# Performance work log

Measured on AMD Instinct MI355X. Metric: run time of the kernel, lower is better.

Reference implementation:

```python
import jax, jax.numpy as jnp
import numpy as np
import math

IN_FEATURES = 4096
OUT_FEATURES = 4096
NUM_COMPONENTS = 256
TWO_PI = 2.0 * math.pi


def setup_inputs() -> dict:
    key = jax.random.key(0)
    k1, k2, k3, k4 = jax.random.split(key, 4)
    x = jax.random.normal(k1, (4096, IN_FEATURES), dtype=jnp.float32)
    mus = jax.random.uniform(k2, (NUM_COMPONENTS, 2), dtype=jnp.float32)
    log_vars = -3.0 - jax.random.uniform(k3, (NUM_COMPONENTS, 2), dtype=jnp.float32)
    weights = jax.random.uniform(k4, (NUM_COMPONENTS,), dtype=jnp.float32) / NUM_COMPONENTS
    return {"x": x, "mus": mus, "log_vars": log_vars, "weights": weights}


def reference(x, mus, log_vars, weights):
    in_features = x.shape[1]
    x_in_idx = jnp.linspace(0.0, 1.0, in_features, dtype=jnp.float32)    # [I]
    x_out_idx = jnp.linspace(0.0, 1.0, OUT_FEATURES, dtype=jnp.float32)  # [O]
    vars_ = jnp.exp(log_vars)  # [M, 2]

    # Input-side Gaussian basis, fused with 1/sqrt(2*pi*var) and component weight: [I, M]
    d_in = (x_in_idx[:, None] - mus[None, :, 0]) ** 2
    G_in = jnp.exp(-d_in / (2.0 * vars_[None, :, 0])) / jnp.sqrt(TWO_PI * vars_[None, :, 0]) * weights[None, :]
    C = x @ G_in  # [B, M]

    # Output-side Gaussian pdf (Normal(mu1, sigma1).log_prob(x_out).exp()): [M, O]
    d_out = (x_out_idx[None, :] - mus[:, 1:2]) ** 2
    G_out = jnp.exp(-d_out / (2.0 * vars_[:, 1:2])) / jnp.sqrt(TWO_PI * vars_[:, 1:2])

    x_out = (C @ G_out) / (in_features * jnp.sum(weights))  # [B, O]
    return x_out
```

## Files before the change

kernel.cpp:

```cpp
#include <hip/hip_runtime.h>
#include <hip/hip_bf16.h>
#include <math.h>

#define IN_FEAT 4096
#define OUT_FEAT 4096
#define NCOMP 256
#define BATCH 4096
#define TWO_PI_F 6.28318530717958647692f

typedef __attribute__((ext_vector_type(8))) short short8;
typedef __attribute__((ext_vector_type(8))) __bf16 bf16x8;
typedef __attribute__((ext_vector_type(4))) float f32x4;
typedef __attribute__((ext_vector_type(16))) float f32x16;

__device__ __forceinline__ ushort f2b(float f) {
  union { float f; unsigned u; } v; v.f = f;
  unsigned r = (v.u + 0x7fffu + ((v.u >> 16) & 1u)) >> 16;
  return (ushort)r;
}

__device__ __forceinline__ float b2f(short s) {
  union { unsigned u; float f; } v; v.u = ((unsigned)(ushort)s) << 16;
  return v.f;
}

__device__ __forceinline__ bf16x8 ld_frag(const void* p) {
  short8 s = *(const short8*)p;
  return __builtin_bit_cast(bf16x8, s);
}

__device__ __forceinline__ short8 cvt8(float4 a, float4 b) {
  short8 h;
  h[0] = (short)f2b(a.x); h[1] = (short)f2b(a.y);
  h[2] = (short)f2b(a.z); h[3] = (short)f2b(a.w);
  h[4] = (short)f2b(b.x); h[5] = (short)f2b(b.y);
  h[6] = (short)f2b(b.z); h[7] = (short)f2b(b.w);
  return h;
}

__device__ __forceinline__ void gload_lds16(const ushort* g, ushort* l) {
  __builtin_amdgcn_global_load_lds(
      (const __attribute__((address_space(1))) void*)g,
      (__attribute__((address_space(3))) void*)l, 16, 0, 0);
}

__global__ __launch_bounds__(256) void prep_kernel(
    const float* __restrict__ mus, const float* __restrict__ lvs,
    const float* __restrict__ w,
    ushort* __restrict__ Gt, ushort* __restrict__ GoT) {
  int idx = blockIdx.x * 256 + threadIdx.x;
  if (idx < NCOMP * IN_FEAT) {
    int m = idx >> 12, i = idx & (IN_FEAT - 1);
    float v = expf(lvs[2 * m]);
    float d = (float)i * (1.0f / (IN_FEAT - 1)) - mus[2 * m];
    float g = expf(-d * d * (0.5f / v)) * rsqrtf(TWO_PI_F * v) * w[m];
    Gt[idx] = f2b(g);
  } else {
    idx -= NCOMP * IN_FEAT;
    int o = idx >> 8, m = idx & (NCOMP - 1);
    float v = expf(lvs[2 * m + 1]);
    float d = (float)o * (1.0f / (OUT_FEAT - 1)) - mus[2 * m + 1];
    float g = expf(-d * d * (0.5f / v)) * rsqrtf(TWO_PI_F * v);
    GoT[idx] = f2b(g);
  }
}

template<int NS>
__global__ __launch_bounds__(256, 4) void gemm1_kernel(
    const float* __restrict__ x, const ushort* __restrict__ Gt,
    ushort* __restrict__ Cpart) {
  constexpr int KR = IN_FEAT / NS;
  constexpr int NT = KR / 32;
  __shared__ __align__(16) ushort lds[2 * 10240];
  const int tid = threadIdx.x, wid = tid >> 6, lane = tid & 63;
  const int m0 = blockIdx.x * 64;
  const int kb0 = blockIdx.y * KR;
  const int r32 = lane & 31, h = lane >> 5;

  f32x16 acc[2][2] = {};

  const int brow = lane >> 2;
  const int bswz = (((lane & 3) ^ ((lane >> 3) & 3)) << 3);
  const int arow = tid >> 2, aslot = tid & 3;
  const float* asrc = &x[(size_t)(m0 + arow) * IN_FEAT + kb0 + aslot * 8];
  const int abyte = arow * 64 + ((aslot << 4) ^ (((arow >> 1) & 3) << 4));
  const int sw0 = (h << 4) ^ (((r32 >> 1) & 3) << 4);

  #define STAGE_B(buf, kb)                                                   \
    _Pragma("unroll")                                                        \
    for (int q = 0; q < 4; ++q) {                                            \
      int nb = wid * 4 + q;                                                  \
      gload_lds16(&Gt[(size_t)(nb * 16 + brow) * IN_FEAT + (kb) + bswz],     \
                  &lds[(buf) * 10240 + nb * 512]);                           \
    }

  {
    float4 a0 = *(const float4*)asrc;
    float4 a1 = *(const float4*)(asrc + 4);
    STAGE_B(0, kb0)
    *(short8*)((char*)lds + 16384 + abyte) = cvt8(a0, a1);
  }
  __syncthreads();

  for (int t = 0; t < NT; ++t) {
    float4 px0, px1;
    if (t + 1 < NT) {
      px0 = *(const float4*)(asrc + (t + 1) * 32);
      px1 = *(const float4*)(asrc + (t + 1) * 32 + 4);
      STAGE_B((t + 1) & 1, kb0 + (t + 1) * 32)
    }
    const char* base = (const char*)lds + (t & 1) * 20480;
    const char* Ab = base + 16384;
    #pragma unroll
    for (int s = 0; s < 2; ++s) {
      const int off = sw0 ^ (s << 5);
      bf16x8 a0 = ld_frag(Ab + r32 * 64 + off);
      bf16x8 a1 = ld_frag(Ab + (32 + r32) * 64 + off);
      bf16x8 b0 = ld_frag(base + (wid * 64 + r32) * 64 + off);
      bf16x8 b1 = ld_frag(base + (wid * 64 + 32 + r32) * 64 + off);
      acc[0][0] = __builtin_amdgcn_mfma_f32_32x32x16_bf16(a0, b0, acc[0][0], 0, 0, 0);
      acc[0][1] = __builtin_amdgcn_mfma_f32_32x32x16_bf16(a0, b1, acc[0][1], 0, 0, 0);
      acc[1][0] = __builtin_amdgcn_mfma_f32_32x32x16_bf16(a1, b0, acc[1][0], 0, 0, 0);
      acc[1][1] = __builtin_amdgcn_mfma_f32_32x32x16_bf16(a1, b1, acc[1][1], 0, 0, 0);
    }
    if (t + 1 < NT)
      *(short8*)((char*)lds + ((t + 1) & 1) * 20480 + 16384 + abyte) =
          cvt8(px0, px1);
    __syncthreads();
  }
  #undef STAGE_B

  ushort* Cp = Cpart + (size_t)blockIdx.y * ((size_t)BATCH * NCOMP);
  #pragma unroll
  for (int mi = 0; mi < 2; ++mi)
    #pragma unroll
    for (int nj = 0; nj < 2; ++nj)
      #pragma unroll
      for (int g = 0; g < 16; ++g) {
        int row = m0 + mi * 32 + (g & 3) + 8 * (g >> 2) + 4 * h;
        int col = wid * 64 + nj * 32 + r32;
        Cp[(size_t)row * NCOMP + col] = f2b(acc[mi][nj][g]);
      }
}

template<int NS>
__global__ __launch_bounds__(256) void reduce_kernel(ushort* __restrict__ Cp) {
  size_t i = ((size_t)blockIdx.x * 256 + threadIdx.x) * 8;
  float s[8] = {};
  #pragma unroll
  for (int p = 0; p < NS; ++p) {
    short8 v = *(const short8*)&Cp[(size_t)p * BATCH * NCOMP + i];
    #pragma unroll
    for (int e = 0; e < 8; ++e) s[e] += b2f(v[e]);
  }
  short8 hh;
  #pragma unroll
  for (int e = 0; e < 8; ++e) hh[e] = (short)f2b(s[e]);
  *(short8*)&Cp[i] = hh;
}

__global__ __launch_bounds__(256, 4) void gemm2_kernel(
    const ushort* __restrict__ Cb, const ushort* __restrict__ GoT,
    const float* __restrict__ w, float* __restrict__ out) {
  __shared__ __align__(16) ushort lds[2 * 8192];
  const int tid = threadIdx.x, wid = tid >> 6, lane = tid & 63;
  const int m0 = blockIdx.y * 128, n0 = blockIdx.x * 128;
  const int wr = (wid >> 1) * 64, wc = (wid & 1) * 64;
  const int r32 = lane & 31, h = lane >> 5;

  float4 wv = *(const float4*)&w[lane * 4];
  float s = wv.x + wv.y + wv.z + wv.w;
  #pragma unroll
  for (int off = 32; off > 0; off >>= 1) s += __shfl_xor(s, off);
  const float scale = 1.0f / ((float)IN_FEAT * s);

  const int brow = lane >> 2;
  const int bswz = (((lane & 3) ^ ((lane >> 3) & 3)) << 3);
  const int sw0 = (h << 4) ^ (((r32 >> 1) & 3) << 4);

  f32x16 acc[2][2] = {};

  #define STAGE2(buf, k0)                                                    \
    _Pragma("unroll")                                                        \
    for (int q = 0; q < 2; ++q) {                                            \
      int c = wid * 2 + q;                                                   \
      int row = c * 16 + brow;                                               \
      gload_lds16(&Cb[(size_t)(m0 + row) * NCOMP + (k0) + bswz],             \
                  &lds[(buf) * 8192 + c * 512]);                             \
      gload_lds16(&GoT[(size_t)(n0 + row) * NCOMP + (k0) + bswz],            \
                  &lds[(buf) * 8192 + 4096 + c * 512]);                      \
    }

  STAGE2(0, 0)
  __syncthreads();

  for (int t = 0; t < 8; ++t) {
    if (t < 7) STAGE2((t + 1) & 1, (t + 1) * 32)
    const char* base = (const char*)lds + (t & 1) * 16384;
    const char* Bb = base + 8192;
    #pragma unroll
    for (int s2 = 0; s2 < 2; ++s2) {
      const int off = sw0 ^ (s2 << 5);
      bf16x8 a0 = ld_frag(base + (wr + r32) * 64 + off);
      bf16x8 a1 = ld_frag(base + (wr + 32 + r32) * 64 + off);
      bf16x8 b0 = ld_frag(Bb + (wc + r32) * 64 + off);
      bf16x8 b1 = ld_frag(Bb + (wc + 32 + r32) * 64 + off);
      acc[0][0] = __builtin_amdgcn_mfma_f32_32x32x16_bf16(a0, b0, acc[0][0], 0, 0, 0);
      acc[0][1] = __builtin_amdgcn_mfma_f32_32x32x16_bf16(a0, b1, acc[0][1], 0, 0, 0);
      acc[1][0] = __builtin_amdgcn_mfma_f32_32x32x16_bf16(a1, b0, acc[1][0], 0, 0, 0);
      acc[1][1] = __builtin_amdgcn_mfma_f32_32x32x16_bf16(a1, b1, acc[1][1], 0, 0, 0);
    }
    __syncthreads();
  }
  #undef STAGE2

  #pragma unroll
  for (int mi = 0; mi < 2; ++mi)
    #pragma unroll
    for (int nj = 0; nj < 2; ++nj)
      #pragma unroll
      for (int g = 0; g < 16; ++g) {
        int row = m0 + wr + mi * 32 + (g & 3) + 8 * (g >> 2) + 4 * h;
        int col = n0 + wc + nj * 32 + r32;
        out[(size_t)row * OUT_FEAT + col] = acc[mi][nj][g] * scale;
      }
}

extern "C" void kernel_launch(void* const* d_in, const int* in_sizes, int n_in,
                              void* d_out, int out_size, void* d_ws, size_t ws_size,
                              hipStream_t stream) {
  const float* x   = (const float*)d_in[0];
  const float* mus = (const float*)d_in[1];
  const float* lvs = (const float*)d_in[2];
  const float* w   = (const float*)d_in[3];
  float* out = (float*)d_out;

  ushort* Gt  = (ushort*)d_ws;
  ushort* GoT = Gt  + (size_t)NCOMP * IN_FEAT;
  ushort* Cpart = GoT + (size_t)OUT_FEAT * NCOMP;

  const size_t MiB = 1024 * 1024;
  int nsplit = 16;
  while (nsplit > 1 && ws_size < 4 * MiB + (size_t)nsplit * 2 * MiB) nsplit >>= 1;

  prep_kernel<<<(NCOMP * IN_FEAT + OUT_FEAT * NCOMP) / 256, 256, 0, stream>>>(
      mus, lvs, w, Gt, GoT);

  dim3 g1(BATCH / 64, nsplit);
  switch (nsplit) {
    case 16: gemm1_kernel<16><<<g1, 256, 0, stream>>>(x, Gt, Cpart);
             reduce_kernel<16><<<BATCH * NCOMP / 8 / 256, 256, 0, stream>>>(Cpart);
             break;
    case 8:  gemm1_kernel<8><<<g1, 256, 0, stream>>>(x, Gt, Cpart);
             reduce_kernel<8><<<BATCH * NCOMP / 8 / 256, 256, 0, stream>>>(Cpart);
             break;
    case 4:  gemm1_kernel<4><<<g1, 256, 0, stream>>>(x, Gt, Cpart);
             reduce_kernel<4><<<BATCH * NCOMP / 8 / 256, 256, 0, stream>>>(Cpart);
             break;
    case 2:  gemm1_kernel<2><<<g1, 256, 0, stream>>>(x, Gt, Cpart);
             reduce_kernel<2><<<BATCH * NCOMP / 8 / 256, 256, 0, stream>>>(Cpart);
             break;
    default: gemm1_kernel<1><<<g1, 256, 0, stream>>>(x, Gt, Cpart);
             break;
  }

  gemm2_kernel<<<dim3(OUT_FEAT / 128, BATCH / 128), 256, 0, stream>>>(
      Cpart, GoT, w, out);
}
```

Measured before the change: 62.14 us.

## Load x fragments directly to registers and software-pipeline gemm1 with vmcnt barriers

The first GEMM no longer stages the fp32 activations through LDS. Each lane loads its own MFMA A-fragment rows straight from global memory into registers and converts them to bf16 just before the MFMAs. The loop is unrolled by two with ping-pong register and LDS buffers, and it waits on partial vmcnt so the next tile's loads overlap the current compute. The K split drops from 16 to 8 and the occupancy hint from 4 to 2, trading less partial-sum traffic for more registers per wave and fewer blocks.

```diff
diff --git a/kernel.cpp b/kernel.cpp
--- a/kernel.cpp
+++ b/kernel.cpp
@@ -29,13 +29,13 @@
   return __builtin_bit_cast(bf16x8, s);
 }
 
-__device__ __forceinline__ short8 cvt8(float4 a, float4 b) {
+__device__ __forceinline__ bf16x8 cvt8(float4 a, float4 b) {
   short8 h;
   h[0] = (short)f2b(a.x); h[1] = (short)f2b(a.y);
   h[2] = (short)f2b(a.z); h[3] = (short)f2b(a.w);
   h[4] = (short)f2b(b.x); h[5] = (short)f2b(b.y);
   h[6] = (short)f2b(b.z); h[7] = (short)f2b(b.w);
-  return h;
+  return __builtin_bit_cast(bf16x8, h);
 }
 
 __device__ __forceinline__ void gload_lds16(const ushort* g, ushort* l) {
@@ -66,69 +66,93 @@
 }
 
 template<int NS>
-__global__ __launch_bounds__(256, 4) void gemm1_kernel(
+__global__ __launch_bounds__(256, 2) void gemm1_kernel(
     const float* __restrict__ x, const ushort* __restrict__ Gt,
     ushort* __restrict__ Cpart) {
   constexpr int KR = IN_FEAT / NS;
   constexpr int NT = KR / 32;
-  __shared__ __align__(16) ushort lds[2 * 10240];
+  __shared__ __align__(16) ushort Bs[2 * 8192];
   const int tid = threadIdx.x, wid = tid >> 6, lane = tid & 63;
+  const int r32 = lane & 31, h = lane >> 5;
   const int m0 = blockIdx.x * 64;
   const int kb0 = blockIdx.y * KR;
-  const int r32 = lane & 31, h = lane >> 5;
 
   f32x16 acc[2][2] = {};
 
   const int brow = lane >> 2;
   const int bswz = (((lane & 3) ^ ((lane >> 3) & 3)) << 3);
-  const int arow = tid >> 2, aslot = tid & 3;
-  const float* asrc = &x[(size_t)(m0 + arow) * IN_FEAT + kb0 + aslot * 8];
-  const int abyte = arow * 64 + ((aslot << 4) ^ (((arow >> 1) & 3) << 4));
   const int sw0 = (h << 4) ^ (((r32 >> 1) & 3) << 4);
+
+  const float* xlo = &x[(size_t)(m0 + r32) * IN_FEAT + kb0 + h * 8];
+  const float* xhi = xlo + (size_t)32 * IN_FEAT;
 
   #define STAGE_B(buf, kb)                                                   \
     _Pragma("unroll")                                                        \
     for (int q = 0; q < 4; ++q) {                                            \
       int nb = wid * 4 + q;                                                  \
       gload_lds16(&Gt[(size_t)(nb * 16 + brow) * IN_FEAT + (kb) + bswz],     \
-                  &lds[(buf) * 10240 + nb * 512]);                           \
+                  &Bs[(buf) * 8192 + nb * 512]);                             \
     }
 
-  {
-    float4 a0 = *(const float4*)asrc;
-    float4 a1 = *(const float4*)(asrc + 4);
-    STAGE_B(0, kb0)
-    *(short8*)((char*)lds + 16384 + abyte) = cvt8(a0, a1);
-  }
-  __syncthreads();
-
-  for (int t = 0; t < NT; ++t) {
-    float4 px0, px1;
-    if (t + 1 < NT) {
-      px0 = *(const float4*)(asrc + (t + 1) * 32);
-      px1 = *(const float4*)(asrc + (t + 1) * 32 + 4);
-      STAGE_B((t + 1) & 1, kb0 + (t + 1) * 32)
-    }
-    const char* base = (const char*)lds + (t & 1) * 20480;
-    const char* Ab = base + 16384;
-    #pragma unroll
-    for (int s = 0; s < 2; ++s) {
-      const int off = sw0 ^ (s << 5);
-      bf16x8 a0 = ld_frag(Ab + r32 * 64 + off);
-      bf16x8 a1 = ld_frag(Ab + (32 + r32) * 64 + off);
-      bf16x8 b0 = ld_frag(base + (wid * 64 + r32) * 64 + off);
-      bf16x8 b1 = ld_frag(base + (wid * 64 + 32 + r32) * 64 + off);
-      acc[0][0] = __builtin_amdgcn_mfma_f32_32x32x16_bf16(a0, b0, acc[0][0], 0, 0, 0);
-      acc[0][1] = __builtin_amdgcn_mfma_f32_32x32x16_bf16(a0, b1, acc[0][1], 0, 0, 0);
-      acc[1][0] = __builtin_amdgcn_mfma_f32_32x32x16_bf16(a1, b0, acc[1][0], 0, 0, 0);
-      acc[1][1] = __builtin_amdgcn_mfma_f32_32x32x16_bf16(a1, b1, acc[1][1], 0, 0, 0);
-    }
-    if (t + 1 < NT)
-      *(short8*)((char*)lds + ((t + 1) & 1) * 20480 + 16384 + abyte) =
-          cvt8(px0, px1);
-    __syncthreads();
-  }
+  #define LOAD_A(px, K)                                                      \
+    px[0] = *(const float4*)(xlo + (K));                                     \
+    px[1] = *(const float4*)(xlo + (K) + 4);                                 \
+    px[2] = *(const float4*)(xlo + (K) + 16);                                \
+    px[3] = *(const float4*)(xlo + (K) + 20);                                \
+    px[4] = *(const float4*)(xhi + (K));                                     \
+    px[5] = *(const float4*)(xhi + (K) + 4);                                 \
+    px[6] = *(const float4*)(xhi + (K) + 16);                                \
+    px[7] = *(const float4*)(xhi + (K) + 20);
+
+  #define COMPUTE(px, buf) {                                                 \
+    const char* Bb = (const char*)&Bs[(buf) * 8192];                         \
+    bf16x8 al0 = cvt8(px[0], px[1]), al1 = cvt8(px[2], px[3]);               \
+    bf16x8 ah0 = cvt8(px[4], px[5]), ah1 = cvt8(px[6], px[7]);               \
+    bf16x8 b00 = ld_frag(Bb + (wid * 64 + r32) * 64 + (sw0 ^ 0));            \
+    bf16x8 b10 = ld_frag(Bb + (wid * 64 + 32 + r32) * 64 + (sw0 ^ 0));       \
+    bf16x8 b01 = ld_frag(Bb + (wid * 64 + r32) * 64 + (sw0 ^ 32));           \
+    bf16x8 b11 = ld_frag(Bb + (wid * 64 + 32 + r32) * 64 + (sw0 ^ 32));      \
+    acc[0][0] = __builtin_amdgcn_mfma_f32_32x32x16_bf16(al0, b00, acc[0][0], 0, 0, 0); \
+    acc[0][1] = __builtin_amdgcn_mfma_f32_32x32x16_bf16(al0, b10, acc[0][1], 0, 0, 0); \
+    acc[1][0] = __builtin_amdgcn_mfma_f32_32x32x16_bf16(ah0, b00, acc[1][0], 0, 0, 0); \
+    acc[1][1] = __builtin_amdgcn_mfma_f32_32x32x16_bf16(ah0, b10, acc[1][1], 0, 0, 0); \
+    acc[0][0] = __builtin_amdgcn_mfma_f32_32x32x16_bf16(al1, b01, acc[0][0], 0, 0, 0); \
+    acc[0][1] = __builtin_amdgcn_mfma_f32_32x32x16_bf16(al1, b11, acc[0][1], 0, 0, 0); \
+    acc[1][0] = __builtin_amdgcn_mfma_f32_32x32x16_bf16(ah1, b01, acc[1][0], 0, 0, 0); \
+    acc[1][1] = __builtin_amdgcn_mfma_f32_32x32x16_bf16(ah1, b11, acc[1][1], 0, 0, 0); }
+
+  #define BAR_V8()                                                           \
+    asm volatile("s_waitcnt vmcnt(8)" ::: "memory");                         \
+    __builtin_amdgcn_s_barrier();                                            \
+    __builtin_amdgcn_sched_barrier(0);
+
+  float4 pe[8], po[8];
+
+  STAGE_B(0, kb0)
+  LOAD_A(pe, 0)
+  BAR_V8()
+
+  int t = 0;
+  for (; t + 1 < NT - 1; t += 2) {
+    STAGE_B(1, kb0 + (t + 1) * 32)
+    LOAD_A(po, (t + 1) * 32)
+    COMPUTE(pe, 0)
+    BAR_V8()
+    STAGE_B(0, kb0 + (t + 2) * 32)
+    LOAD_A(pe, (t + 2) * 32)
+    COMPUTE(po, 1)
+    BAR_V8()
+  }
+  STAGE_B(1, kb0 + (t + 1) * 32)
+  LOAD_A(po, (t + 1) * 32)
+  COMPUTE(pe, 0)
+  BAR_V8()
+  COMPUTE(po, 1)
+
   #undef STAGE_B
+  #undef LOAD_A
+  #undef COMPUTE
+  #undef BAR_V8
 
   ushort* Cp = Cpart + (size_t)blockIdx.y * ((size_t)BATCH * NCOMP);
   #pragma unroll
@@ -240,7 +264,7 @@
   ushort* Cpart = GoT + (size_t)OUT_FEAT * NCOMP;
 
   const size_t MiB = 1024 * 1024;
-  int nsplit = 16;
+  int nsplit = 8;
   while (nsplit > 1 && ws_size < 4 * MiB + (size_t)nsplit * 2 * MiB) nsplit >>= 1;
 
   prep_kernel<<<(NCOMP * IN_FEAT + OUT_FEAT * NCOMP) / 256, 256, 0, stream>>>(
@@ -248,9 +272,6 @@
 
   dim3 g1(BATCH / 64, nsplit);
   switch (nsplit) {
-    case 16: gemm1_kernel<16><<<g1, 256, 0, stream>>>(x, Gt, Cpart);
-             reduce_kernel<16><<<BATCH * NCOMP / 8 / 256, 256, 0, stream>>>(Cpart);
-             break;
     case 8:  gemm1_kernel<8><<<g1, 256, 0, stream>>>(x, Gt, Cpart);
              reduce_kernel<8><<<BATCH * NCOMP / 8 / 256, 256, 0, stream>>>(Cpart);
              break;
```

Result: slower. 78.50 us (+26.3%).

## Restructure gemm1 with triple-buffered async LDS loads of fp32 x and N-split tiles

Applied to the files above, without the earlier changes.

Rewrites the first GEMM so both the fp32 x tile and the bf16 Gt tile are fetched straight into LDS with global_load_lds, in a three-stage ring buffer synchronised by explicit vmcnt waits and barriers. The fp32-to-bf16 conversion of x now happens after reading from LDS instead of going through registers before the store. Each block now covers 128 of the N columns, adding a grid dimension, and the split-K factor drops from 16 to 8. This is meant to overlap memory latency with MFMA work and shrink the partial-sum buffer and reduction traffic, at the cost of doubled LDS bytes for the fp32 A tile, more conversion work per tile, and fewer blocks per CU.

```diff
diff --git a/kernel.cpp b/kernel.cpp
--- a/kernel.cpp
+++ b/kernel.cpp
@@ -29,16 +29,14 @@
   return __builtin_bit_cast(bf16x8, s);
 }
 
-__device__ __forceinline__ short8 cvt8(float4 a, float4 b) {
-  short8 h;
-  h[0] = (short)f2b(a.x); h[1] = (short)f2b(a.y);
-  h[2] = (short)f2b(a.z); h[3] = (short)f2b(a.w);
-  h[4] = (short)f2b(b.x); h[5] = (short)f2b(b.y);
-  h[6] = (short)f2b(b.z); h[7] = (short)f2b(b.w);
-  return h;
-}
-
-__device__ __forceinline__ void gload_lds16(const ushort* g, ushort* l) {
+__device__ __forceinline__ bf16x8 cvt8f(float4 a, float4 b) {
+  bf16x8 r;
+  r[0] = (__bf16)a.x; r[1] = (__bf16)a.y; r[2] = (__bf16)a.z; r[3] = (__bf16)a.w;
+  r[4] = (__bf16)b.x; r[5] = (__bf16)b.y; r[6] = (__bf16)b.z; r[7] = (__bf16)b.w;
+  return r;
+}
+
+__device__ __forceinline__ void gload_lds16(const void* g, void* l) {
   __builtin_amdgcn_global_load_lds(
       (const __attribute__((address_space(1))) void*)g,
       (__attribute__((address_space(3))) void*)l, 16, 0, 0);
@@ -66,81 +64,110 @@
 }
 
 template<int NS>
-__global__ __launch_bounds__(256, 4) void gemm1_kernel(
+__global__ __launch_bounds__(256, 3) void gemm1_kernel(
     const float* __restrict__ x, const ushort* __restrict__ Gt,
     ushort* __restrict__ Cpart) {
   constexpr int KR = IN_FEAT / NS;
   constexpr int NT = KR / 32;
-  __shared__ __align__(16) ushort lds[2 * 10240];
+  __shared__ __align__(16) ushort lds[3 * 8192];
   const int tid = threadIdx.x, wid = tid >> 6, lane = tid & 63;
+  const int r32 = lane & 31, h = lane >> 5;
   const int m0 = blockIdx.x * 64;
-  const int kb0 = blockIdx.y * KR;
-  const int r32 = lane & 31, h = lane >> 5;
-
-  f32x16 acc[2][2] = {};
-
-  const int brow = lane >> 2;
-  const int bswz = (((lane & 3) ^ ((lane >> 3) & 3)) << 3);
-  const int arow = tid >> 2, aslot = tid & 3;
-  const float* asrc = &x[(size_t)(m0 + arow) * IN_FEAT + kb0 + aslot * 8];
-  const int abyte = arow * 64 + ((aslot << 4) ^ (((arow >> 1) & 3) << 4));
-  const int sw0 = (h << 4) ^ (((r32 >> 1) & 3) << 4);
-
-  #define STAGE_B(buf, kb)                                                   \
+  const int n0 = blockIdx.y * 128;
+  const int kb0 = blockIdx.z * KR;
+  const int wr = wid >> 1, wc = wid & 1;
+
+  f32x16 acc[2] = {};
+
+  const char* gp[4];
+  int dofs[4];
+  int gstride;
+  if (wid < 2) {
+    gstride = 128;
+    int row8 = lane >> 3, slin = (lane >> 1) & 3, q16 = lane & 1;
+    int slot = slin ^ (row8 & 3);
+    int kofs = (slot >> 1) * 16 + (slot & 1) * 8 + q16 * 4;
+    #pragma unroll
+    for (int q = 0; q < 4; ++q) {
+      int c = wid * 4 + q;
+      gp[q] = (const char*)&x[(size_t)(m0 + c * 8 + row8) * IN_FEAT + kb0 + kofs];
+      dofs[q] = c * 1024 + lane * 16;
+    }
+  } else {
+    gstride = 64;
+    int col16 = lane >> 2, slin = lane & 3;
+    int slot = slin ^ (col16 & 3);
+    int kofs = (slot >> 1) * 16 + (slot & 1) * 8;
+    #pragma unroll
+    for (int q = 0; q < 4; ++q) {
+      int c = (wid - 2) * 4 + q;
+      gp[q] = (const char*)&Gt[(size_t)(n0 + c * 16 + col16) * IN_FEAT + kb0 + kofs];
+      dofs[q] = 8192 + c * 1024 + lane * 16;
+    }
+  }
+
+  #define STAGE(wb_) {                                                       \
+    char* lb = (char*)lds + (wb_) * 16384;                                   \
     _Pragma("unroll")                                                        \
     for (int q = 0; q < 4; ++q) {                                            \
-      int nb = wid * 4 + q;                                                  \
-      gload_lds16(&Gt[(size_t)(nb * 16 + brow) * IN_FEAT + (kb) + bswz],     \
-                  &lds[(buf) * 10240 + nb * 512]);                           \
-    }
-
-  {
-    float4 a0 = *(const float4*)asrc;
-    float4 a1 = *(const float4*)(asrc + 4);
-    STAGE_B(0, kb0)
-    *(short8*)((char*)lds + 16384 + abyte) = cvt8(a0, a1);
-  }
-  __syncthreads();
-
-  for (int t = 0; t < NT; ++t) {
-    float4 px0, px1;
-    if (t + 1 < NT) {
-      px0 = *(const float4*)(asrc + (t + 1) * 32);
-      px1 = *(const float4*)(asrc + (t + 1) * 32 + 4);
-      STAGE_B((t + 1) & 1, kb0 + (t + 1) * 32)
-    }
-    const char* base = (const char*)lds + (t & 1) * 20480;
-    const char* Ab = base + 16384;
-    #pragma unroll
-    for (int s = 0; s < 2; ++s) {
-      const int off = sw0 ^ (s << 5);
-      bf16x8 a0 = ld_frag(Ab + r32 * 64 + off);
-      bf16x8 a1 = ld_frag(Ab + (32 + r32) * 64 + off);
-      bf16x8 b0 = ld_frag(base + (wid * 64 + r32) * 64 + off);
-      bf16x8 b1 = ld_frag(base + (wid * 64 + 32 + r32) * 64 + off);
-      acc[0][0] = __builtin_amdgcn_mfma_f32_32x32x16_bf16(a0, b0, acc[0][0], 0, 0, 0);
-      acc[0][1] = __builtin_amdgcn_mfma_f32_32x32x16_bf16(a0, b1, acc[0][1], 0, 0, 0);
-      acc[1][0] = __builtin_amdgcn_mfma_f32_32x32x16_bf16(a1, b0, acc[1][0], 0, 0, 0);
-      acc[1][1] = __builtin_amdgcn_mfma_f32_32x32x16_bf16(a1, b1, acc[1][1], 0, 0, 0);
-    }
-    if (t + 1 < NT)
-      *(short8*)((char*)lds + ((t + 1) & 1) * 20480 + 16384 + abyte) =
-          cvt8(px0, px1);
-    __syncthreads();
-  }
-  #undef STAGE_B
-
-  ushort* Cp = Cpart + (size_t)blockIdx.y * ((size_t)BATCH * NCOMP);
-  #pragma unroll
-  for (int mi = 0; mi < 2; ++mi)
-    #pragma unroll
-    for (int nj = 0; nj < 2; ++nj)
-      #pragma unroll
-      for (int g = 0; g < 16; ++g) {
-        int row = m0 + mi * 32 + (g & 3) + 8 * (g >> 2) + 4 * h;
-        int col = wid * 64 + nj * 32 + r32;
-        Cp[(size_t)row * NCOMP + col] = f2b(acc[mi][nj][g]);
-      }
+      gload_lds16(gp[q], lb + dofs[q]);                                      \
+      gp[q] += gstride;                                                      \
+    } }
+
+  const int aswz = r32 & 3;
+  #define COMPUTE(rb_) {                                                     \
+    const char* sb = (const char*)lds + (rb_) * 16384;                       \
+    _Pragma("unroll")                                                        \
+    for (int s = 0; s < 2; ++s) {                                            \
+      const int sa = (s * 2 + h) ^ aswz;                                     \
+      const char* ap = sb + (wr * 32 + r32) * 128 + sa * 32;                 \
+      float4 f0 = *(const float4*)ap;                                        \
+      float4 f1 = *(const float4*)(ap + 16);                                 \
+      bf16x8 af = cvt8f(f0, f1);                                             \
+      _Pragma("unroll")                                                      \
+      for (int nj = 0; nj < 2; ++nj) {                                       \
+        const char* bp = sb + 8192 + ((wc * 2 + nj) * 32 + r32) * 64 + sa * 16; \
+        bf16x8 bf = ld_frag(bp);                                             \
+        acc[nj] = __builtin_amdgcn_mfma_f32_32x32x16_bf16(af, bf, acc[nj], 0, 0, 0); \
+      }                                                                      \
+    } }
+
+  #define WAITBAR(n)                                                         \
+    asm volatile("s_waitcnt vmcnt(" #n ")" ::: "memory");                    \
+    __builtin_amdgcn_s_barrier();                                            \
+    __builtin_amdgcn_sched_barrier(0);
+
+  STAGE(0)
+  STAGE(1)
+
+  int rb = 0, wb = 2;
+  for (int t = 0; t < NT - 2; ++t) {
+    WAITBAR(4)
+    STAGE(wb)
+    COMPUTE(rb)
+    rb = (rb == 2) ? 0 : rb + 1;
+    wb = (wb == 2) ? 0 : wb + 1;
+  }
+  WAITBAR(4)
+  COMPUTE(rb)
+  rb = (rb == 2) ? 0 : rb + 1;
+  WAITBAR(0)
+  COMPUTE(rb)
+
+  #undef STAGE
+  #undef COMPUTE
+  #undef WAITBAR
+
+  ushort* Cp = Cpart + (size_t)blockIdx.z * ((size_t)BATCH * NCOMP);
+  #pragma unroll
+  for (int nj = 0; nj < 2; ++nj) {
+    int col = n0 + wc * 64 + nj * 32 + r32;
+    #pragma unroll
+    for (int g = 0; g < 16; ++g) {
+      int row = m0 + wr * 32 + (g & 3) + 8 * (g >> 2) + 4 * h;
+      Cp[(size_t)row * NCOMP + col] = f2b(acc[nj][g]);
+    }
+  }
 }
 
 template<int NS>
@@ -240,28 +267,28 @@
   ushort* Cpart = GoT + (size_t)OUT_FEAT * NCOMP;
 
   const size_t MiB = 1024 * 1024;
-  int nsplit = 16;
+  int nsplit = 8;
   while (nsplit > 1 && ws_size < 4 * MiB + (size_t)nsplit * 2 * MiB) nsplit >>= 1;
 
   prep_kernel<<<(NCOMP * IN_FEAT + OUT_FEAT * NCOMP) / 256, 256, 0, stream>>>(
       mus, lvs, w, Gt, GoT);
 
-  dim3 g1(BATCH / 64, nsplit);
   switch (nsplit) {
-    case 16: gemm1_kernel<16><<<g1, 256, 0, stream>>>(x, Gt, Cpart);
-             reduce_kernel<16><<<BATCH * NCOMP / 8 / 256, 256, 0, stream>>>(Cpart);
-             break;
-    case 8:  gemm1_kernel<8><<<g1, 256, 0, stream>>>(x, Gt, Cpart);
-             reduce_kernel<8><<<BATCH * NCOMP / 8 / 256, 256, 0, stream>>>(Cpart);
-             break;
-    case 4:  gemm1_kernel<4><<<g1, 256, 0, stream>>>(x, Gt, Cpart);
-             reduce_kernel<4><<<BATCH * NCOMP / 8 / 256, 256, 0, stream>>>(Cpart);
-             break;
-    case 2:  gemm1_kernel<2><<<g1, 256, 0, stream>>>(x, Gt, Cpart);
-             reduce_kernel<2><<<BATCH * NCOMP / 8 / 256, 256, 0, stream>>>(Cpart);
-             break;
-    default: gemm1_kernel<1><<<g1, 256, 0, stream>>>(x, Gt, Cpart);
-             break;
+    case 8:
+      gemm1_kernel<8><<<dim3(BATCH / 64, 2, 8), 256, 0, stream>>>(x, Gt, Cpart);
+      reduce_kernel<8><<<BATCH * NCOMP / 8 / 256, 256, 0, stream>>>(Cpart);
+      break;
+    case 4:
+      gemm1_kernel<4><<<dim3(BATCH / 64, 2, 4), 256, 0, stream>>>(x, Gt, Cpart);
+      reduce_kernel<4><<<BATCH * NCOMP / 8 / 256, 256, 0, stream>>>(Cpart);
+      break;
+    case 2:
+      gemm1_kernel<2><<<dim3(BATCH / 64, 2, 2), 256, 0, stream>>>(x, Gt, Cpart);
+      reduce_kernel<2><<<BATCH * NCOMP / 8 / 256, 256, 0, stream>>>(Cpart);
+      break;
+    default:
+      gemm1_kernel<1><<<dim3(BATCH / 64, 2, 1), 256, 0, stream>>>(x, Gt, Cpart);
+      break;
   }
 
   gemm2_kernel<<<dim3(OUT_FEAT / 128, BATCH / 128), 256, 0, stream>>>(
```

New measurement: 77.73 us. 25.1% more time.
